# Kernel tuning notes

Hardware: AMD Instinct MI355X
Metric: run time of the kernel (lower is better)

Reference implementation:

```python
import jax, jax.numpy as jnp
import numpy as np

N_ATOMS = 20000        # nodes
N_EDGES = 400000       # avg degree 20
C = 4                  # num_pseudo_species channels
F_IN = 128             # ps_input_size
CONV = [64, 64]        # conv_sizes
HID = [64, 32]         # hidden_sizes
OUT = 1                # output_size (energy)
N_STRUCT = 32          # structures in batch
AVG_ATOMS = 20.0       # average_number_of_atoms
NEG_SLOPE = 0.2        # GAT leaky_relu slope


def setup_inputs() -> dict:
    key = jax.random.key(0)
    ks = jax.random.split(key, 16)
    x = jax.random.normal(ks[0], (N_ATOMS, C, F_IN), dtype=jnp.float32)
    edge_index = jax.random.randint(ks[1], (2, N_EDGES), 0, N_ATOMS)
    batch_ids = jnp.sort(jax.random.randint(ks[2], (N_ATOMS,), 0, N_STRUCT))

    def w(k, shape, fan_in):
        return jax.random.normal(k, shape, dtype=jnp.float32) / np.float32(np.sqrt(fan_in))

    return {
        "x": x,
        "edge_index": edge_index,
        "batch_ids": batch_ids,
        "gamma": jnp.ones((F_IN,), jnp.float32),
        "beta": jnp.zeros((F_IN,), jnp.float32),
        # MultiChannelGATConv 1: F_IN -> 64
        "Wc1": w(ks[3], (C, F_IN, CONV[0]), F_IN),
        "asrc1": w(ks[4], (C, CONV[0]), CONV[0]),
        "adst1": w(ks[5], (C, CONV[0]), CONV[0]),
        # MultiChannelGATConv 2: 64 -> 64
        "Wc2": w(ks[6], (C, CONV[0], CONV[1]), CONV[0]),
        "asrc2": w(ks[7], (C, CONV[1]), CONV[1]),
        "adst2": w(ks[8], (C, CONV[1]), CONV[1]),
        # MultiChannelLinear MLP: 64 -> 64 -> 32
        "Wn1": w(ks[9], (C, CONV[1], HID[0]), CONV[1]),
        "Wn2": w(ks[10], (C, HID[0], HID[1]), HID[0]),
        # out_linear: 32 -> 1
        "Wout": w(ks[11], (C, HID[1], OUT), HID[1]),
    }


def _layer_norm(x, gamma, beta):
    mu = jnp.mean(x, axis=-1, keepdims=True)
    var = jnp.mean((x - mu) ** 2, axis=-1, keepdims=True)
    return (x - mu) * jax.lax.rsqrt(var + 1e-5) * gamma + beta


def _gat_conv(x, W, a_src, a_dst, src, dst):
    # per-channel GATConv (single head, no bias): x [N,C,Fin] -> [N,C,Fout]
    h = jnp.einsum('ncf,cfo->nco', x, W)                       # [N,C,Fout]
    e_src = jnp.einsum('nco,co->nc', h, a_src)                 # [N,C]
    e_dst = jnp.einsum('nco,co->nc', h, a_dst)                 # [N,C]
    logit = jax.nn.leaky_relu(e_src[src] + e_dst[dst], NEG_SLOPE)  # [E,C]
    m = jax.ops.segment_max(logit, dst, num_segments=N_ATOMS)      # [N,C]
    ex = jnp.exp(logit - m[dst])                                   # [E,C]
    den = jax.ops.segment_sum(ex, dst, num_segments=N_ATOMS)       # [N,C]
    alpha = ex / (den[dst] + 1e-16)                                # [E,C]
    msg = alpha[:, :, None] * h[src]                               # [E,C,Fout]
    return jax.ops.segment_sum(msg, dst, num_segments=N_ATOMS)     # [N,C,Fout]


def reference(x, edge_index, batch_ids, gamma, beta,
              Wc1, asrc1, adst1, Wc2, asrc2, adst2,
              Wn1, Wn2, Wout):
    src, dst = edge_index[0], edge_index[1]
    h = _layer_norm(x, gamma, beta)
    h = jax.nn.silu(_gat_conv(h, Wc1, asrc1, adst1, src, dst))
    h = jax.nn.silu(_gat_conv(h, Wc2, asrc2, adst2, src, dst))
    h = jax.nn.silu(jnp.einsum('ncf,cfo->nco', h, Wn1))
    h = jax.nn.silu(jnp.einsum('ncf,cfo->nco', h, Wn2))
    h = jnp.einsum('ncf,cfo->nco', h, Wout)                    # [N,C,1]
    feats = jnp.sum(h, axis=1)                                  # sum_over_components -> [N,1]
    energies = jax.ops.segment_sum(feats, batch_ids, num_segments=N_STRUCT)  # [S,1]
    energies = energies / jnp.sqrt(jnp.float32(C))
    energies = energies / jnp.float32(AVG_ATOMS)
    return energies
```

## Files before the change

### kernel.cpp

```cpp
#include <hip/hip_runtime.h>
#include <hip/hip_bf16.h>
#include <hip/hip_fp16.h>

#define N_ATOMS 20000
#define N_EDGES 400000
#define NCH 4
#define F_IN 128
#define S_OUT 32

__device__ __forceinline__ float silu_f(float v) { return v / (1.f + __expf(-v)); }

typedef _Float16 half8v __attribute__((ext_vector_type(8)));
typedef float f32x4v __attribute__((ext_vector_type(4)));

__device__ __forceinline__ half8v ld_frag(const __half* p) {
    union { float4 f; half8v h; } u;
    u.f = *(const float4*)p;
    return u.h;
}

__device__ __forceinline__ int wave_iscan(int v, int l) {
#pragma unroll
    for (int off = 1; off < 64; off <<= 1) {
        int t = __shfl_up(v, off);
        if (l >= off) v += t;
    }
    return v;
}

__global__ void fill_kernel(float* __restrict__ p, int n, float v) {
    int i = blockIdx.x * blockDim.x + threadIdx.x;
    int stride = gridDim.x * blockDim.x;
    for (; i < n; i += stride) p[i] = v;
}

__global__ void hist_kernel(const int* __restrict__ ei, int* __restrict__ cnt, int E) {
    int e = blockIdx.x * 256 + threadIdx.x;
    if (e < E) atomicAdd(&cnt[ei[E + e]], 1);
}

__global__ __launch_bounds__(256) void scan_l1_kernel(const int* __restrict__ cnt,
                                                      int* __restrict__ rowp,
                                                      int* __restrict__ bsum, int n) {
    int i = blockIdx.x * 256 + threadIdx.x;
    int l = threadIdx.x & 63, w = threadIdx.x >> 6;
    int v = (i < n) ? cnt[i] : 0;
    int incl = wave_iscan(v, l);
    __shared__ int wsum[4];
    if (l == 63) wsum[w] = incl;
    __syncthreads();
    int add = 0;
#pragma unroll
    for (int j = 0; j < 4; ++j) add += (j < w) ? wsum[j] : 0;
    if (i < n) rowp[i] = add + incl - v;
    if (threadIdx.x == 255) bsum[blockIdx.x] = add + incl;
}

__global__ __launch_bounds__(256) void scan_l2_kernel(const int* __restrict__ bsum,
                                                      int* __restrict__ boff,
                                                      int* __restrict__ rowp_n, int nb,
                                                      float* __restrict__ out_zero) {
    int i = threadIdx.x;
    if (i < S_OUT) out_zero[i] = 0.f;
    int l = i & 63, w = i >> 6;
    int v = (i < nb) ? bsum[i] : 0;
    int incl = wave_iscan(v, l);
    __shared__ int wsum[4];
    if (l == 63) wsum[w] = incl;
    __syncthreads();
    int add = 0;
#pragma unroll
    for (int j = 0; j < 4; ++j) add += (j < w) ? wsum[j] : 0;
    if (i < nb) boff[i] = add + incl - v;
    if (i == nb - 1) *rowp_n = add + incl;
}

__global__ __launch_bounds__(256) void scan_l3_kernel(int* __restrict__ rowp,
                                                      const int* __restrict__ boff, int n) {
    int i = blockIdx.x * 256 + threadIdx.x;
    if (i < n) rowp[i] += boff[blockIdx.x];
}

__global__ void scatter_kernel(const int* __restrict__ ei, const int* __restrict__ rowp,
                               int* __restrict__ fill, int* __restrict__ csr_src, int E) {
    int e = blockIdx.x * 256 + threadIdx.x;
    if (e < E) {
        int d = ei[E + e];
        int pos = rowp[d] + atomicAdd(&fill[d], 1);
        csr_src[pos] = ei[e];
    }
}

template <int FIN, int IN_STRIDE, bool IN_HALF, bool LN, bool ATT, bool SILU_OUT, bool OUT_HALF>
__global__ __launch_bounds__(256) void proj_kernel(const void* __restrict__ inv,
                                                   const float* __restrict__ gamma,
                                                   const float* __restrict__ beta,
                                                   const float* __restrict__ W,
                                                   const float* __restrict__ a_src,
                                                   const float* __restrict__ a_dst,
                                                   void* __restrict__ outv,
                                                   float* __restrict__ es,
                                                   float* __restrict__ ed) {
    constexpr int OCT = FIN / 8;
    constexpr int OM = OCT - 1;
    constexpr int WSH = FIN + 8;
    __shared__ __half Wt[64 * WSH];
    __shared__ __half inl[64 * WSH];
    const int tid = threadIdx.x;
    const int c = blockIdx.y;
    const int n0 = blockIdx.x * 64;
    const int w = tid >> 6;
    const int l = tid & 63;
    const int col = l & 15;
    const int g = l >> 4;

    const float* __restrict__ Wc = W + c * (FIN * 64);
    for (int i = tid; i < (FIN / 2) * 64; i += 256) {
        int kp = i >> 6, oo = i & 63;
        int k = kp * 2;
        float w0 = Wc[(size_t)k * 64 + oo];
        float w1 = Wc[(size_t)(k + 1) * 64 + oo];
        int pos = ((((k >> 3) ^ (oo >> 2)) & OM) << 3) | (k & 7);
        *(__half2*)(&Wt[oo * WSH + pos]) = __floats2half2_rn(w0, w1);
    }
    if (IN_HALF) {
        const __half* __restrict__ inh = (const __half*)inv;
        for (int i = tid; i < 64 * (FIN / 8); i += 256) {
            int nl = i / (FIN / 8), ch = i % (FIN / 8);
            int node = min(n0 + nl, N_ATOMS - 1);
            *(float4*)(inl + nl * WSH + ch * 8) =
                *(const float4*)(inh + (size_t)node * IN_STRIDE + c * FIN + ch * 8);
        }
    } else {
        const float* __restrict__ inf = (const float*)inv;
        for (int i = tid; i < 64 * (FIN / 8); i += 256) {
            int nl = i / (FIN / 8), ch = i % (FIN / 8);
            int node = min(n0 + nl, N_ATOMS - 1);
            const float* src = inf + (size_t)node * IN_STRIDE + c * FIN + ch * 8;
            float4 a = *(const float4*)src;
            float4 b = *(const float4*)(src + 4);
            float4 st;
            __half2* sp = (__half2*)&st;
            sp[0] = __floats2half2_rn(a.x, a.y);
            sp[1] = __floats2half2_rn(a.z, a.w);
            sp[2] = __floats2half2_rn(b.x, b.y);
            sp[3] = __floats2half2_rn(b.z, b.w);
            *(float4*)(inl + nl * WSH + ch * 8) = st;
        }
    }
    __syncthreads();

    if (LN) {
        int sub = l >> 4;
        int l16 = l & 15;
        float gv[8], bv8[8];
#pragma unroll
        for (int j = 0; j < 8; ++j) {
            gv[j] = gamma[l16 * 8 + j];
            bv8[j] = beta[l16 * 8 + j];
        }
#pragma unroll
        for (int it = 0; it < 4; ++it) {
            int row = w * 16 + it * 4 + sub;
            __half* rp = inl + row * WSH + l16 * 8;
            float4 raw = *(const float4*)rp;
            __half2* hp = (__half2*)&raw;
            float v[8];
#pragma unroll
            for (int j = 0; j < 4; ++j) {
                float2 f = __half22float2(hp[j]);
                v[2 * j] = f.x;
                v[2 * j + 1] = f.y;
            }
            float s = 0.f, sq = 0.f;
#pragma unroll
            for (int j = 0; j < 8; ++j) { s += v[j]; sq += v[j] * v[j]; }
#pragma unroll
            for (int off = 1; off < 16; off <<= 1) {
                s += __shfl_xor(s, off);
                sq += __shfl_xor(sq, off);
            }
            float mu = s * (1.f / 128.f);
            float rs = rsqrtf(sq * (1.f / 128.f) - mu * mu + 1e-5f);
            float4 st;
            __half2* sp = (__half2*)&st;
#pragma unroll
            for (int j = 0; j < 4; ++j)
                sp[j] = __floats2half2_rn((v[2 * j] - mu) * rs * gv[2 * j] + bv8[2 * j],
                                          (v[2 * j + 1] - mu) * rs * gv[2 * j + 1] + bv8[2 * j + 1]);
            *(float4*)rp = st;
        }
        __syncthreads();
    }

    f32x4v acc[4];
#pragma unroll
    for (int t = 0; t < 4; ++t) acc[t] = (f32x4v){0.f, 0.f, 0.f, 0.f};

    const __half* arow = inl + (w * 16 + col) * WSH + g * 8;
#pragma unroll
    for (int it = 0; it < FIN / 32; ++it) {
        half8v af = ld_frag(arow + it * 32);
        int J = it * 4 + g;
#pragma unroll
        for (int t = 0; t < 4; ++t) {
            int oo = 16 * t + col;
            half8v bf = ld_frag(Wt + oo * WSH + (((J ^ (oo >> 2)) & OM) << 3));
            acc[t] = __builtin_amdgcn_mfma_f32_16x16x32_f16(af, bf, acc[t], 0, 0, 0);
        }
    }

    float av[4], bv[4];
    if (ATT) {
#pragma unroll
        for (int t = 0; t < 4; ++t) {
            av[t] = a_src[c * 64 + 16 * t + col];
            bv[t] = a_dst[c * 64 + 16 * t + col];
        }
    }
#pragma unroll
    for (int r = 0; r < 4; ++r) {
        int node = n0 + w * 16 + g * 4 + r;
        bool valid = node < N_ATOMS;
        if (valid) {
#pragma unroll
            for (int t = 0; t < 4; ++t) {
                float o = acc[t][r];
                if (SILU_OUT) o = silu_f(o);
                if (OUT_HALF)
                    ((__half*)outv)[(size_t)node * 256 + c * 64 + 16 * t + col] = __float2half(o);
                else
                    ((float*)outv)[(size_t)node * 256 + c * 64 + 16 * t + col] = o;
            }
        }
        if (ATT) {
            float ps = 0.f, pd = 0.f;
#pragma unroll
            for (int t = 0; t < 4; ++t) {
                ps = fmaf(acc[t][r], av[t], ps);
                pd = fmaf(acc[t][r], bv[t], pd);
            }
#pragma unroll
            for (int off = 1; off < 16; off <<= 1) {
                ps += __shfl_xor(ps, off);
                pd += __shfl_xor(pd, off);
            }
            if (col == 0 && valid) { es[node * NCH + c] = ps; ed[node * NCH + c] = pd; }
        }
    }
}

__global__ __launch_bounds__(256) void gat_gather_kernel(const int* __restrict__ rowp,
                                                         const int* __restrict__ csr_src,
                                                         const float* __restrict__ es,
                                                         const float* __restrict__ ed,
                                                         const __half* __restrict__ h,
                                                         __half* __restrict__ out) {
    int l = threadIdx.x & 63;
    int d = blockIdx.x * 4 + (threadIdx.x >> 6);
    int c = l >> 4, q = l & 15;
    int r0 = rowp[d], r1 = rowp[d + 1];
    float edc = ed[d * NCH + c];
    float m = -1e30f, den = 0.f;
    float a0 = 0.f, a1 = 0.f, a2 = 0.f, a3 = 0.f;
    int grp = l & 48;

    for (int base = r0; base < r1; base += 16) {
        int len = min(16, r1 - base);
        float logit = -1e30f;
        int s = 0;
        if (q < len) {
            s = csr_src[base + q];
            float v = es[s * NCH + c] + edc;
            logit = v >= 0.f ? v : 0.2f * v;
        }
        float cm = logit;
#pragma unroll
        for (int off = 8; off; off >>= 1) cm = fmaxf(cm, __shfl_xor(cm, off));
        float nm = fmaxf(m, cm);
        float resc = __expf(m - nm);
        float ex = (q < len) ? __expf(logit - nm) : 0.f;
        float cs = ex;
#pragma unroll
        for (int off = 8; off; off >>= 1) cs += __shfl_xor(cs, off);
        den = den * resc + cs;
        a0 *= resc; a1 *= resc; a2 *= resc; a3 *= resc;
        m = nm;
        int e = 0;
        for (; e + 4 <= len; e += 4) {
            int s0 = __shfl(s, e),     s1 = __shfl(s, e + 1);
            int s2 = __shfl(s, e + 2), s3 = __shfl(s, e + 3);
            float x0 = __shfl(ex, grp | e),       x1 = __shfl(ex, grp | (e + 1));
            float x2 = __shfl(ex, grp | (e + 2)), x3 = __shfl(ex, grp | (e + 3));
            float2 hv0 = *(const float2*)(h + (size_t)s0 * 256 + l * 4);
            float2 hv1 = *(const float2*)(h + (size_t)s1 * 256 + l * 4);
            float2 hv2 = *(const float2*)(h + (size_t)s2 * 256 + l * 4);
            float2 hv3 = *(const float2*)(h + (size_t)s3 * 256 + l * 4);
            __half2* p0 = (__half2*)&hv0;
            __half2* p1 = (__half2*)&hv1;
            __half2* p2 = (__half2*)&hv2;
            __half2* p3 = (__half2*)&hv3;
            float2 f00 = __half22float2(p0[0]), f01 = __half22float2(p0[1]);
            float2 f10 = __half22float2(p1[0]), f11 = __half22float2(p1[1]);
            float2 f20 = __half22float2(p2[0]), f21 = __half22float2(p2[1]);
            float2 f30 = __half22float2(p3[0]), f31 = __half22float2(p3[1]);
            a0 = fmaf(x0, f00.x, fmaf(x1, f10.x, fmaf(x2, f20.x, fmaf(x3, f30.x, a0))));
            a1 = fmaf(x0, f00.y, fmaf(x1, f10.y, fmaf(x2, f20.y, fmaf(x3, f30.y, a1))));
            a2 = fmaf(x0, f01.x, fmaf(x1, f11.x, fmaf(x2, f21.x, fmaf(x3, f31.x, a2))));
            a3 = fmaf(x0, f01.y, fmaf(x1, f11.y, fmaf(x2, f21.y, fmaf(x3, f31.y, a3))));
        }
        for (; e < len; ++e) {
            int se = __shfl(s, e);
            float xe = __shfl(ex, grp | e);
            float2 hv = *(const float2*)(h + (size_t)se * 256 + l * 4);
            __half2* hp = (__half2*)&hv;
            float2 f0 = __half22float2(hp[0]), f1 = __half22float2(hp[1]);
            a0 = fmaf(xe, f0.x, a0);
            a1 = fmaf(xe, f0.y, a1);
            a2 = fmaf(xe, f1.x, a2);
            a3 = fmaf(xe, f1.y, a3);
        }
    }
    float inv = 1.f / (den + 1e-16f);
    float2 st;
    __half2* sp = (__half2*)&st;
    sp[0] = __floats2half2_rn(silu_f(a0 * inv), silu_f(a1 * inv));
    sp[1] = __floats2half2_rn(silu_f(a2 * inv), silu_f(a3 * inv));
    *(float2*)(out + (size_t)d * 256 + l * 4) = st;
}

__global__ __launch_bounds__(256) void mlp_fused_kernel(const __half* __restrict__ in,
                                                        const float* __restrict__ W1,
                                                        const float* __restrict__ W2,
                                                        const float* __restrict__ W3,
                                                        const int* __restrict__ bat,
                                                        float* __restrict__ out) {
    constexpr int WSH = 72;
    __shared__ __half W1t[64 * WSH];
    __shared__ __half inl[64 * WSH];
    __shared__ __half t1l[64 * WSH];
    __shared__ __half W2t[NCH][32 * WSH];
    __shared__ float w3l[NCH * 32];
    __shared__ float ynode[64];
    const int tid = threadIdx.x;
    const int n0 = blockIdx.x * 64;
    const int w = tid >> 6;
    const int l = tid & 63;
    const int col = l & 15;
    const int g = l >> 4;

    for (int i = tid; i < NCH * 32 * 32; i += 256) {
        int cc = i >> 10, rem = i & 1023;
        int kp = rem >> 5, o2 = rem & 31;
        int k = kp * 2;
        float a = W2[cc * 2048 + k * 32 + o2];
        float b = W2[cc * 2048 + (k + 1) * 32 + o2];
        int pos = ((((k >> 3) ^ (o2 >> 2)) & 7) << 3) | (k & 7);
        *(__half2*)(&W2t[cc][o2 * WSH + pos]) = __floats2half2_rn(a, b);
    }
    if (tid < NCH * 32) w3l[tid] = W3[tid];

    float yacc[4] = {0.f, 0.f, 0.f, 0.f};

    for (int c = 0; c < NCH; ++c) {
        __syncthreads();
        for (int i = tid; i < 32 * 64; i += 256) {
            int kp = i >> 6, oo = i & 63;
            int k = kp * 2;
            float a = W1[c * 4096 + k * 64 + oo];
            float b = W1[c * 4096 + (k + 1) * 64 + oo];
            int pos = ((((k >> 3) ^ (oo >> 2)) & 7) << 3) | (k & 7);
            *(__half2*)(&W1t[oo * WSH + pos]) = __floats2half2_rn(a, b);
        }
        for (int i = tid; i < 64 * 8; i += 256) {
            int nl = i >> 3, ch = i & 7;
            int node = min(n0 + nl, N_ATOMS - 1);
            *(float4*)(inl + nl * WSH + ch * 8) =
                *(const float4*)(in + (size_t)node * 256 + c * 64 + ch * 8);
        }
        __syncthreads();

        f32x4v acc[4];
#pragma unroll
        for (int t = 0; t < 4; ++t) acc[t] = (f32x4v){0.f, 0.f, 0.f, 0.f};
        const __half* arow = inl + (w * 16 + col) * WSH + g * 8;
#pragma unroll
        for (int it = 0; it < 2; ++it) {
            half8v af = ld_frag(arow + it * 32);
            int J = it * 4 + g;
#pragma unroll
            for (int t = 0; t < 4; ++t) {
                int oo = 16 * t + col;
                half8v bf = ld_frag(W1t + oo * WSH + (((J ^ (oo >> 2)) & 7) << 3));
                acc[t] = __builtin_amdgcn_mfma_f32_16x16x32_f16(af, bf, acc[t], 0, 0, 0);
            }
        }
#pragma unroll
        for (int t = 0; t < 4; ++t)
#pragma unroll
            for (int r = 0; r < 4; ++r)
                t1l[(w * 16 + g * 4 + r) * WSH + 16 * t + col] = __float2half(silu_f(acc[t][r]));

        f32x4v acc2[2];
        acc2[0] = (f32x4v){0.f, 0.f, 0.f, 0.f};
        acc2[1] = (f32x4v){0.f, 0.f, 0.f, 0.f};
        const __half* arow2 = t1l + (w * 16 + col) * WSH + g * 8;
#pragma unroll
        for (int it = 0; it < 2; ++it) {
            half8v af = ld_frag(arow2 + it * 32);
            int J = it * 4 + g;
#pragma unroll
            for (int t = 0; t < 2; ++t) {
                int o2 = 16 * t + col;
                half8v bf = ld_frag(&W2t[c][o2 * WSH + (((J ^ (o2 >> 2)) & 7) << 3)]);
                acc2[t] = __builtin_amdgcn_mfma_f32_16x16x32_f16(af, bf, acc2[t], 0, 0, 0);
            }
        }
        float w3a = w3l[c * 32 + col], w3b = w3l[c * 32 + 16 + col];
#pragma unroll
        for (int r = 0; r < 4; ++r) {
            float p = silu_f(acc2[0][r]) * w3a + silu_f(acc2[1][r]) * w3b;
#pragma unroll
            for (int off = 1; off < 16; off <<= 1) p += __shfl_xor(p, off);
            yacc[r] += p;
        }
    }

    if (col == 0) {
#pragma unroll
        for (int r = 0; r < 4; ++r) ynode[w * 16 + g * 4 + r] = yacc[r];
    }
    __syncthreads();
    if (tid < 64) {
        int node = n0 + tid;
        bool act = node < N_ATOMS;
        float val = act ? ynode[tid] * 0.025f : 0.f;
        int b = act ? bat[min(node, N_ATOMS - 1)] : 0;
        unsigned long long rem = __ballot(act);
        while (rem) {
            int lead = (int)__ffsll(rem) - 1;
            int bl = __shfl(b, lead);
            bool mine = act && (b == bl);
            float t = mine ? val : 0.f;
#pragma unroll
            for (int off = 32; off; off >>= 1) t += __shfl_xor(t, off);
            if (tid == lead) atomicAdd(out + bl, t);
            rem &= ~__ballot(mine);
        }
    }
}

extern "C" void kernel_launch(void* const* d_in, const int* in_sizes, int n_in,
                              void* d_out, int out_size, void* d_ws, size_t ws_size,
                              hipStream_t stream) {
    const float* x     = (const float*)d_in[0];
    const int*   ei    = (const int*)d_in[1];
    const int*   bat   = (const int*)d_in[2];
    const float* gamma = (const float*)d_in[3];
    const float* beta  = (const float*)d_in[4];
    const float* Wc1   = (const float*)d_in[5];
    const float* as1   = (const float*)d_in[6];
    const float* ad1   = (const float*)d_in[7];
    const float* Wc2   = (const float*)d_in[8];
    const float* as2   = (const float*)d_in[9];
    const float* ad2   = (const float*)d_in[10];
    const float* Wn1   = (const float*)d_in[11];
    const float* Wn2   = (const float*)d_in[12];
    const float* Wout  = (const float*)d_in[13];
    float* out = (float*)d_out;

    float* A    = (float*)d_ws;
    float* B    = A + 10240000;
    float* es   = B + 5120000;
    float* ed   = es + 80000;
    int* rowp   = (int*)(ed + 80000);
    int* cnt    = rowp + 20004;
    int* fillc  = cnt + 20000;
    int* csr    = fillc + 20000;
    int* bsum   = csr + 400000;
    int* boff   = bsum + 128;
    __half* C1h = (__half*)A;
    __half* C2h = (__half*)(A + 2560000);
    __half* Bh  = (__half*)B;

    dim3 blk(256);
    const int NB = (N_ATOMS + 255) / 256;
    const int NT64 = (N_ATOMS + 63) / 64;

    fill_kernel<<<80, blk, 0, stream>>>((float*)cnt, 40000, 0.f);
    hist_kernel<<<(N_EDGES + 255) / 256, blk, 0, stream>>>(ei, cnt, N_EDGES);
    scan_l1_kernel<<<NB, blk, 0, stream>>>(cnt, rowp, bsum, N_ATOMS);
    scan_l2_kernel<<<1, blk, 0, stream>>>(bsum, boff, rowp + N_ATOMS, NB, out);
    scan_l3_kernel<<<NB, blk, 0, stream>>>(rowp, boff, N_ATOMS);
    scatter_kernel<<<(N_EDGES + 255) / 256, blk, 0, stream>>>(ei, rowp, fillc, csr, N_EDGES);

    proj_kernel<128, NCH * F_IN, false, true, true, false, true>
        <<<dim3(NT64, NCH), blk, 0, stream>>>(x, gamma, beta, Wc1, as1, ad1, Bh, es, ed);
    gat_gather_kernel<<<N_ATOMS / 4, blk, 0, stream>>>(rowp, csr, es, ed, Bh, C1h);

    proj_kernel<64, 256, true, false, true, false, true>
        <<<dim3(NT64, NCH), blk, 0, stream>>>(C1h, gamma, beta, Wc2, as2, ad2, Bh, es, ed);
    gat_gather_kernel<<<N_ATOMS / 4, blk, 0, stream>>>(rowp, csr, es, ed, Bh, C2h);

    mlp_fused_kernel<<<NT64, blk, 0, stream>>>(C2h, Wn1, Wn2, Wout, bat, out);
}
```

Measured before the change: 175.0 us.

## Store GAT features channel-major and split gather across channels via grid.y

Intermediate node features move from a node-major [N,C,64] layout to a channel-major [C,N,64] layout across both projection kernels, both gather kernels and the MLP. The gather kernel now launches one block row per channel, and each wave processes four edges at a time in parallel across 16-lane groups, then reduces the partial sums with cross-lane shuffles. The goal is to raise gather parallelism and keep each channel's feature table (about 2.5 MB) cache-resident. The cost is four times as many gather blocks, each re-reading the CSR row and edge indices, plus extra shuffle reductions.

```diff
diff --git a/kernel.cpp b/kernel.cpp
--- a/kernel.cpp
+++ b/kernel.cpp
@@ -91,7 +91,8 @@
     }
 }
 
-template <int FIN, int IN_STRIDE, bool IN_HALF, bool LN, bool ATT, bool SILU_OUT, bool OUT_HALF>
+template <int FIN, int IN_STRIDE, bool IN_HALF, bool IN_CMAJ, bool LN, bool ATT,
+          bool SILU_OUT, bool OUT_HALF, bool OUT_CMAJ>
 __global__ __launch_bounds__(256) void proj_kernel(const void* __restrict__ inv,
                                                    const float* __restrict__ gamma,
                                                    const float* __restrict__ beta,
@@ -128,8 +129,10 @@
         for (int i = tid; i < 64 * (FIN / 8); i += 256) {
             int nl = i / (FIN / 8), ch = i % (FIN / 8);
             int node = min(n0 + nl, N_ATOMS - 1);
-            *(float4*)(inl + nl * WSH + ch * 8) =
-                *(const float4*)(inh + (size_t)node * IN_STRIDE + c * FIN + ch * 8);
+            const __half* src = IN_CMAJ
+                ? inh + ((size_t)c * N_ATOMS + node) * 64 + ch * 8
+                : inh + (size_t)node * IN_STRIDE + c * FIN + ch * 8;
+            *(float4*)(inl + nl * WSH + ch * 8) = *(const float4*)src;
         }
     } else {
         const float* __restrict__ inf = (const float*)inv;
@@ -227,10 +230,12 @@
             for (int t = 0; t < 4; ++t) {
                 float o = acc[t][r];
                 if (SILU_OUT) o = silu_f(o);
+                size_t idx = OUT_CMAJ ? ((size_t)c * N_ATOMS + node) * 64 + 16 * t + col
+                                      : (size_t)node * 256 + c * 64 + 16 * t + col;
                 if (OUT_HALF)
-                    ((__half*)outv)[(size_t)node * 256 + c * 64 + 16 * t + col] = __float2half(o);
+                    ((__half*)outv)[idx] = __float2half(o);
                 else
-                    ((float*)outv)[(size_t)node * 256 + c * 64 + 16 * t + col] = o;
+                    ((float*)outv)[idx] = o;
             }
         }
         if (ATT) {
@@ -258,12 +263,15 @@
                                                          __half* __restrict__ out) {
     int l = threadIdx.x & 63;
     int d = blockIdx.x * 4 + (threadIdx.x >> 6);
-    int c = l >> 4, q = l & 15;
+    int c = blockIdx.y;
+    int q = l & 15;
+    int g = l >> 4;
+    int grp = l & 48;
+    const __half* __restrict__ hc = h + (size_t)c * N_ATOMS * 64;
     int r0 = rowp[d], r1 = rowp[d + 1];
     float edc = ed[d * NCH + c];
     float m = -1e30f, den = 0.f;
     float a0 = 0.f, a1 = 0.f, a2 = 0.f, a3 = 0.f;
-    int grp = l & 48;
 
     for (int base = r0; base < r1; base += 16) {
         int len = min(16, r1 - base);
@@ -286,33 +294,15 @@
         den = den * resc + cs;
         a0 *= resc; a1 *= resc; a2 *= resc; a3 *= resc;
         m = nm;
-        int e = 0;
-        for (; e + 4 <= len; e += 4) {
-            int s0 = __shfl(s, e),     s1 = __shfl(s, e + 1);
-            int s2 = __shfl(s, e + 2), s3 = __shfl(s, e + 3);
-            float x0 = __shfl(ex, grp | e),       x1 = __shfl(ex, grp | (e + 1));
-            float x2 = __shfl(ex, grp | (e + 2)), x3 = __shfl(ex, grp | (e + 3));
-            float2 hv0 = *(const float2*)(h + (size_t)s0 * 256 + l * 4);
-            float2 hv1 = *(const float2*)(h + (size_t)s1 * 256 + l * 4);
-            float2 hv2 = *(const float2*)(h + (size_t)s2 * 256 + l * 4);
-            float2 hv3 = *(const float2*)(h + (size_t)s3 * 256 + l * 4);
-            __half2* p0 = (__half2*)&hv0;
-            __half2* p1 = (__half2*)&hv1;
-            __half2* p2 = (__half2*)&hv2;
-            __half2* p3 = (__half2*)&hv3;
-            float2 f00 = __half22float2(p0[0]), f01 = __half22float2(p0[1]);
-            float2 f10 = __half22float2(p1[0]), f11 = __half22float2(p1[1]);
-            float2 f20 = __half22float2(p2[0]), f21 = __half22float2(p2[1]);
-            float2 f30 = __half22float2(p3[0]), f31 = __half22float2(p3[1]);
-            a0 = fmaf(x0, f00.x, fmaf(x1, f10.x, fmaf(x2, f20.x, fmaf(x3, f30.x, a0))));
-            a1 = fmaf(x0, f00.y, fmaf(x1, f10.y, fmaf(x2, f20.y, fmaf(x3, f30.y, a1))));
-            a2 = fmaf(x0, f01.x, fmaf(x1, f11.x, fmaf(x2, f21.x, fmaf(x3, f31.x, a2))));
-            a3 = fmaf(x0, f01.y, fmaf(x1, f11.y, fmaf(x2, f21.y, fmaf(x3, f31.y, a3))));
-        }
-        for (; e < len; ++e) {
-            int se = __shfl(s, e);
-            float xe = __shfl(ex, grp | e);
-            float2 hv = *(const float2*)(h + (size_t)se * 256 + l * 4);
+#pragma unroll
+        for (int j = 0; j < 4; ++j) {
+            int e = g + 4 * j;
+            bool act = e < len;
+            int ee = act ? e : 0;
+            float xe = __shfl(ex, grp | ee);
+            int se = __shfl(s, grp | ee);
+            xe = act ? xe : 0.f;
+            float2 hv = *(const float2*)(hc + (size_t)se * 64 + q * 4);
             __half2* hp = (__half2*)&hv;
             float2 f0 = __half22float2(hp[0]), f1 = __half22float2(hp[1]);
             a0 = fmaf(xe, f0.x, a0);
@@ -321,12 +311,21 @@
             a3 = fmaf(xe, f1.y, a3);
         }
     }
-    float inv = 1.f / (den + 1e-16f);
-    float2 st;
-    __half2* sp = (__half2*)&st;
-    sp[0] = __floats2half2_rn(silu_f(a0 * inv), silu_f(a1 * inv));
-    sp[1] = __floats2half2_rn(silu_f(a2 * inv), silu_f(a3 * inv));
-    *(float2*)(out + (size_t)d * 256 + l * 4) = st;
+#pragma unroll
+    for (int off = 16; off < 64; off <<= 1) {
+        a0 += __shfl_xor(a0, off);
+        a1 += __shfl_xor(a1, off);
+        a2 += __shfl_xor(a2, off);
+        a3 += __shfl_xor(a3, off);
+    }
+    if (g == 0) {
+        float inv = 1.f / (den + 1e-16f);
+        float2 st;
+        __half2* sp = (__half2*)&st;
+        sp[0] = __floats2half2_rn(silu_f(a0 * inv), silu_f(a1 * inv));
+        sp[1] = __floats2half2_rn(silu_f(a2 * inv), silu_f(a3 * inv));
+        *(float2*)(out + ((size_t)c * N_ATOMS + d) * 64 + q * 4) = st;
+    }
 }
 
 __global__ __launch_bounds__(256) void mlp_fused_kernel(const __half* __restrict__ in,
@@ -376,7 +375,7 @@
             int nl = i >> 3, ch = i & 7;
             int node = min(n0 + nl, N_ATOMS - 1);
             *(float4*)(inl + nl * WSH + ch * 8) =
-                *(const float4*)(in + (size_t)node * 256 + c * 64 + ch * 8);
+                *(const float4*)(in + ((size_t)c * N_ATOMS + node) * 64 + ch * 8);
         }
         __syncthreads();
 
@@ -494,13 +493,13 @@
     scan_l3_kernel<<<NB, blk, 0, stream>>>(rowp, boff, N_ATOMS);
     scatter_kernel<<<(N_EDGES + 255) / 256, blk, 0, stream>>>(ei, rowp, fillc, csr, N_EDGES);
 
-    proj_kernel<128, NCH * F_IN, false, true, true, false, true>
+    proj_kernel<128, NCH * F_IN, false, false, true, true, false, true, true>
         <<<dim3(NT64, NCH), blk, 0, stream>>>(x, gamma, beta, Wc1, as1, ad1, Bh, es, ed);
-    gat_gather_kernel<<<N_ATOMS / 4, blk, 0, stream>>>(rowp, csr, es, ed, Bh, C1h);
-
-    proj_kernel<64, 256, true, false, true, false, true>
+    gat_gather_kernel<<<dim3(N_ATOMS / 4, NCH), blk, 0, stream>>>(rowp, csr, es, ed, Bh, C1h);
+
+    proj_kernel<64, 64, true, true, false, true, false, true, true>
         <<<dim3(NT64, NCH), blk, 0, stream>>>(C1h, gamma, beta, Wc2, as2, ad2, Bh, es, ed);
-    gat_gather_kernel<<<N_ATOMS / 4, blk, 0, stream>>>(rowp, csr, es, ed, Bh, C2h);
+    gat_gather_kernel<<<dim3(N_ATOMS / 4, NCH), blk, 0, stream>>>(rowp, csr, es, ed, Bh, C2h);
 
     mlp_fused_kernel<<<NT64, blk, 0, stream>>>(C2h, Wn1, Wn2, Wout, bat, out);
 }
```

Result: slower. 203.5 us (+16.3%).
